# Optimization experiments

Hardware: AMD Instinct MI355X
Metric: run time of the kernel (lower is better)

## Reference

```python
import jax, jax.numpy as jnp
import numpy as np
from jax import lax

SPARSITY = 0.5  # args.sparsity: fraction of weights KEPT


def get_subnet(scores, k):
    """GetSubnet.forward: sort |scores|, zero lowest (1-k) fraction, one elsewhere."""
    sa = jnp.abs(scores)
    n = sa.size
    j = int((1.0 - k) * n)  # static: number of entries zeroed
    idx = jnp.argsort(sa.ravel())  # ascending, matches torch .sort()
    mask = jnp.zeros((n,), dtype=sa.dtype).at[idx[j:]].set(1.0)
    return mask.reshape(scores.shape)


def masked_conv(x, w, s, b, stride):
    m = get_subnet(s, SPARSITY)
    y = lax.conv_general_dilated(
        x, w * m, window_strides=(stride, stride), padding=((1, 1), (1, 1)),
        dimension_numbers=('NCHW', 'OIHW', 'NCHW'))
    return y + b[None, :, None, None]


def setup_inputs() -> dict:
    key = jax.random.key(0)
    ks = jax.random.split(key, 16)
    def rn(k, shape, scale):
        return jax.random.normal(k, shape, dtype=jnp.float32) * scale
    return {
        'x':   rn(ks[0], (64, 3, 64, 64), 1.0),
        'w1':  rn(ks[1], (128, 3, 3, 3), 0.2),   's1': rn(ks[2], (128, 3, 3, 3), 1.0),   'b1': rn(ks[3], (128,), 0.01),
        'w2':  rn(ks[4], (256, 128, 3, 3), 0.05), 's2': rn(ks[5], (256, 128, 3, 3), 1.0), 'b2': rn(ks[6], (256,), 0.01),
        'w3':  rn(ks[7], (512, 256, 3, 3), 0.03), 's3': rn(ks[8], (512, 256, 3, 3), 1.0), 'b3': rn(ks[9], (512,), 0.01),
        'fw1': rn(ks[10], (1024, 512), 0.05),     'fs1': rn(ks[11], (1024, 512), 1.0),    'fb1': rn(ks[12], (1024,), 0.01),
        'fw2': rn(ks[13], (10, 1024), 0.05),      'fs2': rn(ks[14], (10, 1024), 1.0),     'fb2': rn(ks[15], (10,), 0.01),
    }


def reference(x, w1, s1, b1, w2, s2, b2, w3, s3, b3, fw1, fs1, fb1, fw2, fs2, fb2):
    h = jax.nn.relu(masked_conv(x, w1, s1, b1, stride=1))   # [64,128,64,64]
    h = jax.nn.relu(masked_conv(h, w2, s2, b2, stride=2))   # [64,256,32,32]
    h = jax.nn.relu(masked_conv(h, w3, s3, b3, stride=2))   # [64,512,16,16]
    h = h.mean(axis=(2, 3))                                 # [64,512] global avg pool
    m1 = get_subnet(fs1, SPARSITY)
    h = jax.nn.relu(h @ (fw1 * m1).T + fb1)                 # [64,1024]
    m2 = get_subnet(fs2, SPARSITY)
    return h @ (fw2 * m2).T + fb2                           # [64,10]
```

## Files before the change

### kernel.cpp

```cpp
#include <hip/hip_runtime.h>
#include <stdint.h>


typedef __attribute__((ext_vector_type(8))) short short8;
typedef __attribute__((ext_vector_type(4))) short short4v;
typedef __attribute__((ext_vector_type(4))) float floatx4;

__device__ __forceinline__ unsigned short f2bf(float f) {
    unsigned u = __float_as_uint(f);
    u += 0x7fffu + ((u >> 16) & 1u);
    return (unsigned short)(u >> 16);
}

constexpr unsigned CUM0 = 3456u;
constexpr unsigned CUM1 = 298368u;
constexpr unsigned CUM2 = 1478016u;
constexpr unsigned CUM3 = 2002304u;
constexpr unsigned STOT = 2012544u;
constexpr int NBH = 512;

__device__ __forceinline__ int find_tensor(unsigned idx, unsigned& li) {
    if (idx < CUM0) { li = idx;        return 0; }
    if (idx < CUM1) { li = idx - CUM0; return 1; }
    if (idx < CUM2) { li = idx - CUM1; return 2; }
    if (idx < CUM3) { li = idx - CUM2; return 3; }
    li = idx - CUM3; return 4;
}

__global__ __launch_bounds__(256) void histfind(const float* __restrict__ s0,
                                                const float* __restrict__ s1,
                                                const float* __restrict__ s2,
                                                const float* __restrict__ s3,
                                                const float* __restrict__ s4,
                                                unsigned* __restrict__ ghist4,
                                                unsigned* __restrict__ done,
                                                unsigned* __restrict__ P,
                                                unsigned* __restrict__ targ,
                                                int pass) {
    __shared__ unsigned lh[4 * 1280];
    __shared__ unsigned sticket;
    const int tid = threadIdx.x;
    const int wv = tid >> 6;
    for (int i = tid; i < 4 * 1280; i += 256) lh[i] = 0;
    __syncthreads();

    const int hi_sh = 31 - 8 * pass;
    const int bin_sh = 23 - 8 * pass;
    unsigned pref[5];
    #pragma unroll
    for (int t = 0; t < 5; t++) pref[t] = pass ? P[t] : 0u;

    for (unsigned idx = blockIdx.x * 256u + tid; idx < STOT; idx += (unsigned)NBH * 256u) {
        unsigned li; int t = find_tensor(idx, li);
        const float* sp = t == 0 ? s0 : t == 1 ? s1 : t == 2 ? s2 : t == 3 ? s3 : s4;
        unsigned key = __float_as_uint(sp[li]) & 0x7fffffffu;
        if ((key >> hi_sh) == pref[t]) {
            unsigned bin = (pass == 3) ? (key & 127u) : ((key >> bin_sh) & 255u);
            atomicAdd(&lh[wv * 1280 + (unsigned)t * 256u + bin], 1u);
        }
    }
    __syncthreads();

    unsigned* gh = ghist4 + pass * 1280;
    for (int i = tid; i < 1280; i += 256) {
        unsigned v = lh[i] + lh[1280 + i] + lh[2560 + i] + lh[3840 + i];
        if (v) atomicAdd(&gh[i], v);
    }
    __syncthreads();
    if (tid == 0) {
        __threadfence();
        sticket = atomicAdd(&done[pass], 1u);
    }
    __syncthreads();

    if (sticket == (unsigned)(NBH - 1)) {
        for (int i = tid; i < 1280; i += 256)
            lh[i] = atomicAdd(&gh[i], 0u);
        __syncthreads();
        if (tid < 5) {
            int t = tid;
            unsigned n = t == 0 ? 3456u : t == 1 ? 294912u : t == 2 ? 1179648u
                       : t == 3 ? 524288u : 10240u;
            unsigned target = (pass == 0) ? (n >> 1) : targ[t];
            const unsigned* bins = &lh[t * 256];
            unsigned cum = 0; int b = 0;
            for (; b < 256; b++) { unsigned c = bins[b]; if (cum + c > target) break; cum += c; }
            targ[t] = target - cum;
            unsigned prev = (pass == 0) ? 0u : P[t];
            P[t] = (prev << ((pass == 3) ? 7 : 8)) | (unsigned)b;
        }
    }
}

__global__ void mask_reorder(const float* __restrict__ w0, const float* __restrict__ w1,
                             const float* __restrict__ w2, const float* __restrict__ w3,
                             const float* __restrict__ w4,
                             const float* __restrict__ s0, const float* __restrict__ s1,
                             const float* __restrict__ s2, const float* __restrict__ s3,
                             const float* __restrict__ s4,
                             const unsigned* __restrict__ T,
                             float* __restrict__ wm1,
                             unsigned short* __restrict__ A2,
                             unsigned short* __restrict__ A3,
                             float* __restrict__ fwm1, float* __restrict__ fwm2,
                             float* __restrict__ pooled) {
    unsigned idx = blockIdx.x * 256u + threadIdx.x;
    if (idx >= STOT) return;
    if (idx < 32768u) pooled[idx] = 0.f;
    unsigned li; int t = find_tensor(idx, li);
    const float* sp = t == 0 ? s0 : t == 1 ? s1 : t == 2 ? s2 : t == 3 ? s3 : s4;
    const float* wp = t == 0 ? w0 : t == 1 ? w1 : t == 2 ? w2 : t == 3 ? w3 : w4;
    unsigned key = __float_as_uint(sp[li]) & 0x7fffffffu;
    float val = (key >= T[t]) ? wp[li] : 0.f;
    if (t == 0) {
        wm1[li] = val;
    } else if (t == 1) {
        unsigned k = li / 1152u, r = li - k * 1152u;
        unsigned c = r / 9u, e = r - c * 9u;
        A2[((size_t)e * 256u + k) * 128u + c] = f2bf(val);
    } else if (t == 2) {
        unsigned k = li / 2304u, r = li - k * 2304u;
        unsigned c = r / 9u, e = r - c * 9u;
        A3[((size_t)e * 512u + k) * 256u + c] = f2bf(val);
    } else if (t == 3) {
        fwm1[li] = val;
    } else {
        fwm2[li] = val;
    }
}

template <int C, int H, int W, int K, int TX, int TY, int KT>
__global__ __launch_bounds__(TX* TY) void conv_direct(const float* __restrict__ in,
                                                      const float* __restrict__ wm,
                                                      const float* __restrict__ bias,
                                                      unsigned short* __restrict__ out) {
    constexpr int TILW = TX * 2, TILH = TY * 2;
    constexpr int ITW = TILW + 2, ITH = TILH + 2;
    constexpr int NTHREADS = TX * TY;
    constexpr int NLOAD = (ITH * ITW + NTHREADS - 1) / NTHREADS;
    constexpr int KG = K / KT;

    __shared__ float sIn[ITH * ITW];
    __shared__ float sW[9 * KT];

    const int tid = threadIdx.x;
    const int tx = tid % TX, ty = tid / TX;
    const int kg = blockIdx.z % KG, n = blockIdx.z / KG;
    const int ox0 = blockIdx.x * TILW, oy0 = blockIdx.y * TILH;
    const int ix0 = ox0 - 1, iy0 = oy0 - 1;

    const float* inN = in + (size_t)n * C * H * W;
    const float* wkg = wm + (size_t)kg * KT * C * 9;

    int goff[NLOAD];
    #pragma unroll
    for (int i = 0; i < NLOAD; i++) {
        int idx = tid + i * NTHREADS;
        if (idx < ITH * ITW) {
            int r = idx / ITW, col = idx % ITW;
            int gy = iy0 + r, gx = ix0 + col;
            goff[i] = (gy >= 0 && gy < H && gx >= 0 && gx < W) ? (gy * W + gx) : -1;
        } else goff[i] = -2;
    }

    float acc[2][2][KT];
    #pragma unroll
    for (int py = 0; py < 2; py++)
        #pragma unroll
        for (int px = 0; px < 2; px++)
            #pragma unroll
            for (int j = 0; j < KT; j++) acc[py][px][j] = 0.f;

    for (int c = 0; c < C; c++) {
        const float* inC = inN + (size_t)c * H * W;
        #pragma unroll
        for (int i = 0; i < NLOAD; i++) {
            int g = goff[i];
            if (g >= -1) sIn[tid + i * NTHREADS] = (g >= 0) ? inC[g] : 0.f;
        }
        for (int i = tid; i < 9 * KT; i += NTHREADS) {
            int e = i / KT, j = i % KT;
            sW[i] = wkg[j * C * 9 + c * 9 + e];
        }
        __syncthreads();

        float vin[4][4];
        const float* base = &sIn[(ty * 2) * ITW + tx * 2];
        #pragma unroll
        for (int r = 0; r < 4; r++)
            #pragma unroll
            for (int cc = 0; cc < 4; cc++) vin[r][cc] = base[r * ITW + cc];

        #pragma unroll
        for (int e = 0; e < 9; e++) {
            const int dy = e / 3, dx = e % 3;
            #pragma unroll
            for (int j = 0; j < KT; j++) {
                float wv = sW[e * KT + j];
                #pragma unroll
                for (int py = 0; py < 2; py++)
                    #pragma unroll
                    for (int px = 0; px < 2; px++)
                        acc[py][px][j] = fmaf(vin[py + dy][px + dx], wv, acc[py][px][j]);
            }
        }
        __syncthreads();
    }

    float bj[KT];
    #pragma unroll
    for (int j = 0; j < KT; j++) bj[j] = bias[kg * KT + j];
    #pragma unroll
    for (int py = 0; py < 2; py++)
        #pragma unroll
        for (int px = 0; px < 2; px++) {
            int oy = oy0 + ty * 2 + py, ox = ox0 + tx * 2 + px;
            short8 v;
            #pragma unroll
            for (int j = 0; j < KT; j++) {
                float t = acc[py][px][j] + bj[j];
                v[j] = (short)f2bf(t > 0.f ? t : 0.f);
            }
            *(short8*)(out + ((size_t)(n * H + oy) * W + ox) * K + kg * KT) = v;
        }
}

template <int C, int H, int W, int KOUT, bool POOL>
__global__ __launch_bounds__(256) void conv_mfma(const unsigned short* __restrict__ in,
                                                 const unsigned short* __restrict__ A,
                                                 const float* __restrict__ bias,
                                                 void* __restrict__ outv) {
    constexpr int OH = H / 2, OW = W / 2;
    constexpr int PR = 128 / OW;
    constexpr int RH = 2 * PR + 1;
    constexpr int IW = W + 1;
    constexpr int NC = C / 32;
    constexpr int PSTR = 40;
    constexpr int NSLOT = RH * IW * 4;
    constexpr int SLMAX = (NSLOT + 255) / 256;

    __shared__ unsigned short sIn[RH * IW * PSTR];

    const int tid = threadIdx.x;
    const int lane = tid & 63;
    const int wv = tid >> 6;
    const int l15 = lane & 15;
    const int quad = lane >> 4;
    const int pt = blockIdx.x, kb = blockIdx.y, n = blockIdx.z;
    const int k0 = kb * 128;
    const int oy0 = pt * PR;
    const int g0y = 2 * oy0 - 1;
    const int mw = wv * 32;

    int goff[SLMAX], slds[SLMAX];
    #pragma unroll
    for (int i = 0; i < SLMAX; i++) {
        int s = tid + i * 256;
        if (s < NSLOT) {
            int q = s & 3, pix = s >> 2;
            int ix = pix % IW, iy = pix / IW;
            int gy = g0y + iy, gx = ix - 1;
            slds[i] = pix * PSTR + q * 8;
            goff[i] = (gy >= 0 && gy < H && gx >= 0) ? ((gy * W + gx) * C + q * 8) : -1;
        } else { goff[i] = -2; slds[i] = 0; }
    }

    int pB[8];
    #pragma unroll
    for (int fn = 0; fn < 8; fn++) {
        int p = fn * 16 + l15;
        int oyl = p / OW, oxl = p % OW;
        pB[fn] = (oyl * 2 * IW + oxl * 2) * PSTR + quad * 8;
    }

    const unsigned short* inN = in + (size_t)n * H * W * C;

    floatx4 acc[2][8];
    #pragma unroll
    for (int fm = 0; fm < 2; fm++)
        #pragma unroll
        for (int fn = 0; fn < 8; fn++) acc[fm][fn] = (floatx4){0.f, 0.f, 0.f, 0.f};

    for (int cc = 0; cc < NC; cc++) {
        __syncthreads();
        const int cof = cc * 32;
        #pragma unroll
        for (int i = 0; i < SLMAX; i++) {
            int g = goff[i];
            if (g >= 0) {
                *(short8*)&sIn[slds[i]] = *(const short8*)(inN + g + cof);
            } else if (g == -1 && cc == 0) {
                *(short8*)&sIn[slds[i]] = (short8){0, 0, 0, 0, 0, 0, 0, 0};
            }
        }
        __syncthreads();

        const unsigned short* Abase = A + (size_t)(k0 + mw + l15) * C + cof + quad * 8;
        const size_t estr = (size_t)KOUT * C;

        short8 a0 = *(const short8*)(Abase);
        short8 a1 = *(const short8*)(Abase + 16 * C);

        #pragma unroll 1
        for (int e = 0; e < 9; e++) {
            short8 ac0 = a0, ac1 = a1;
            if (e < 8) {
                a0 = *(const short8*)(Abase + (size_t)(e + 1) * estr);
                a1 = *(const short8*)(Abase + (size_t)(e + 1) * estr + 16 * C);
            }
            const int dy = e / 3, dx = e - dy * 3;
            const int boff = (dy * IW + dx) * PSTR;
            short8 bfr[8];
            #pragma unroll
            for (int fn = 0; fn < 8; fn++)
                bfr[fn] = *(const short8*)&sIn[pB[fn] + boff];
            #pragma unroll
            for (int fn = 0; fn < 8; fn++) {
                acc[0][fn] = __builtin_amdgcn_mfma_f32_16x16x32_bf16(ac0, bfr[fn], acc[0][fn], 0, 0, 0);
                acc[1][fn] = __builtin_amdgcn_mfma_f32_16x16x32_bf16(ac1, bfr[fn], acc[1][fn], 0, 0, 0);
            }
        }
    }

    if (!POOL) {
        unsigned short* out = (unsigned short*)outv;
        #pragma unroll
        for (int fm = 0; fm < 2; fm++) {
            const int k4 = k0 + mw + fm * 16 + quad * 4;
            float b0 = bias[k4], b1 = bias[k4 + 1], b2 = bias[k4 + 2], b3 = bias[k4 + 3];
            #pragma unroll
            for (int fn = 0; fn < 8; fn++) {
                int p = fn * 16 + l15;
                int oy = oy0 + p / OW, ox = p % OW;
                float v0 = acc[fm][fn][0] + b0, v1 = acc[fm][fn][1] + b1;
                float v2 = acc[fm][fn][2] + b2, v3 = acc[fm][fn][3] + b3;
                short4v v;
                v[0] = (short)f2bf(v0 > 0.f ? v0 : 0.f);
                v[1] = (short)f2bf(v1 > 0.f ? v1 : 0.f);
                v[2] = (short)f2bf(v2 > 0.f ? v2 : 0.f);
                v[3] = (short)f2bf(v3 > 0.f ? v3 : 0.f);
                *(short4v*)(out + ((size_t)(n * OH + oy) * OW + ox) * KOUT + k4) = v;
            }
        }
    } else {
        float* out = (float*)outv;
        #pragma unroll
        for (int fm = 0; fm < 2; fm++) {
            #pragma unroll
            for (int reg = 0; reg < 4; reg++) {
                int k = k0 + mw + fm * 16 + quad * 4 + reg;
                float bv = bias[k];
                float s = 0.f;
                #pragma unroll
                for (int fn = 0; fn < 8; fn++) {
                    float v = acc[fm][fn][reg] + bv;
                    s += v > 0.f ? v : 0.f;
                }
                s += __shfl_xor(s, 1); s += __shfl_xor(s, 2);
                s += __shfl_xor(s, 4); s += __shfl_xor(s, 8);
                if (l15 == 0) atomicAdd(&out[n * KOUT + k], s * (1.0f / (OH * OW)));
            }
        }
    }
}

__global__ __launch_bounds__(256) void fc_fused(const float* __restrict__ pooled,
                                                const float* __restrict__ w1v,
                                                const float* __restrict__ b1v,
                                                const float* __restrict__ w2v,
                                                const float* __restrict__ b2v,
                                                float* __restrict__ out) {
    const int n = blockIdx.x, tid = threadIdx.x;
    __shared__ float sp[512];
    __shared__ float sh[1024];
    __shared__ float redw[40];

    {
        float2 v = *(const float2*)(pooled + (size_t)n * 512 + tid * 2);
        sp[tid * 2] = v.x; sp[tid * 2 + 1] = v.y;
    }
    __syncthreads();

    #pragma unroll
    for (int j = 0; j < 4; j++) {
        int o = tid + j * 256;
        const float4* w4 = (const float4*)(w1v + (size_t)o * 512);
        float acc = 0.f;
        for (int i = 0; i < 128; i++) {
            float4 ww = w4[i];
            acc += sp[i * 4] * ww.x + sp[i * 4 + 1] * ww.y
                 + sp[i * 4 + 2] * ww.z + sp[i * 4 + 3] * ww.w;
        }
        acc += b1v[o];
        sh[o] = acc > 0.f ? acc : 0.f;
    }
    __syncthreads();

    for (int o = 0; o < 10; o++) {
        const float4* w4 = (const float4*)(w2v + (size_t)o * 1024);
        float4 ww = w4[tid];
        float v = sh[tid * 4] * ww.x + sh[tid * 4 + 1] * ww.y
                + sh[tid * 4 + 2] * ww.z + sh[tid * 4 + 3] * ww.w;
        for (int off = 32; off > 0; off >>= 1) v += __shfl_down(v, off);
        if ((tid & 63) == 0) redw[o * 4 + (tid >> 6)] = v;
    }
    __syncthreads();
    if (tid < 10) {
        out[n * 10 + tid] = redw[tid * 4] + redw[tid * 4 + 1]
                          + redw[tid * 4 + 2] + redw[tid * 4 + 3] + b2v[tid];
    }
}

extern "C" void kernel_launch(void* const* d_in, const int* in_sizes, int n_in,
                              void* d_out, int out_size, void* d_ws, size_t ws_size,
                              hipStream_t stream) {
    const float* x   = (const float*)d_in[0];
    const float* w1  = (const float*)d_in[1];
    const float* s1  = (const float*)d_in[2];
    const float* b1  = (const float*)d_in[3];
    const float* w2  = (const float*)d_in[4];
    const float* s2  = (const float*)d_in[5];
    const float* b2  = (const float*)d_in[6];
    const float* w3  = (const float*)d_in[7];
    const float* s3  = (const float*)d_in[8];
    const float* b3  = (const float*)d_in[9];
    const float* fw1 = (const float*)d_in[10];
    const float* fs1 = (const float*)d_in[11];
    const float* fb1 = (const float*)d_in[12];
    const float* fw2 = (const float*)d_in[13];
    const float* fs2 = (const float*)d_in[14];
    const float* fb2 = (const float*)d_in[15];
    float* out = (float*)d_out;

    char* ws = (char*)d_ws;
    size_t off = 0;
    auto alloc = [&](size_t bytes) -> char* {
        char* p = ws + off;
        off = (off + bytes + 255) & ~(size_t)255;
        return p;
    };
    unsigned* ghist = (unsigned*)alloc((4 * 1280 + 16) * 4);
    unsigned* done  = ghist + 4 * 1280;
    unsigned* P     = (unsigned*)alloc(64);
    unsigned* targ  = (unsigned*)alloc(64);
    float* wm1  = (float*)alloc(3456ull * 4);
    float* fwm1 = (float*)alloc(524288ull * 4);
    float* fwm2 = (float*)alloc(10240ull * 4);
    unsigned short* A2 = (unsigned short*)alloc(294912ull * 2);
    unsigned short* A3 = (unsigned short*)alloc(1179648ull * 2);
    unsigned short* h1 = (unsigned short*)alloc(33554432ull * 2);
    unsigned short* h2 = (unsigned short*)alloc(16777216ull * 2);
    float* pooled = (float*)alloc(32768ull * 4);
    if (off > ws_size) return;

    (void)hipMemsetAsync(ghist, 0, (4 * 1280 + 16) * 4, stream);

    for (int pass = 0; pass < 4; pass++)
        histfind<<<NBH, 256, 0, stream>>>(s1, s2, s3, fs1, fs2, ghist, done, P, targ, pass);

    int gs = (STOT + 255) / 256;
    mask_reorder<<<gs, 256, 0, stream>>>(w1, w2, w3, fw1, fw2, s1, s2, s3, fs1, fs2, P,
                                         wm1, A2, A3, fwm1, fwm2, pooled);

    conv_direct<3, 64, 64, 128, 16, 16, 8>
        <<<dim3(2, 2, 64 * 16), 256, 0, stream>>>(x, wm1, b1, h1);
    conv_mfma<128, 64, 64, 256, false>
        <<<dim3(8, 2, 64), 256, 0, stream>>>(h1, A2, b2, h2);
    conv_mfma<256, 32, 32, 512, true>
        <<<dim3(2, 4, 64), 256, 0, stream>>>(h2, A3, b3, pooled);

    fc_fused<<<64, 256, 0, stream>>>(pooled, fwm1, fb1, fwm2, fb2, out);
}
```

Before: 469.3 us.

## Split histogram radix-select into separate hist and find kernels, fewer blocks

After: 482.9 us. 1.03x slower.

```diff
diff --git a/kernel.cpp b/kernel.cpp
--- a/kernel.cpp
+++ b/kernel.cpp
@@ -17,7 +17,7 @@
 constexpr unsigned CUM2 = 1478016u;
 constexpr unsigned CUM3 = 2002304u;
 constexpr unsigned STOT = 2012544u;
-constexpr int NBH = 512;
+constexpr int NBH = 128;
 
 __device__ __forceinline__ int find_tensor(unsigned idx, unsigned& li) {
     if (idx < CUM0) { li = idx;        return 0; }
@@ -27,18 +27,14 @@
     li = idx - CUM3; return 4;
 }
 
-__global__ __launch_bounds__(256) void histfind(const float* __restrict__ s0,
-                                                const float* __restrict__ s1,
-                                                const float* __restrict__ s2,
-                                                const float* __restrict__ s3,
-                                                const float* __restrict__ s4,
-                                                unsigned* __restrict__ ghist4,
-                                                unsigned* __restrict__ done,
-                                                unsigned* __restrict__ P,
-                                                unsigned* __restrict__ targ,
-                                                int pass) {
+__global__ __launch_bounds__(256) void hist8(const float* __restrict__ s0,
+                                             const float* __restrict__ s1,
+                                             const float* __restrict__ s2,
+                                             const float* __restrict__ s3,
+                                             const float* __restrict__ s4,
+                                             const unsigned* __restrict__ P,
+                                             unsigned* __restrict__ ghist4, int pass) {
     __shared__ unsigned lh[4 * 1280];
-    __shared__ unsigned sticket;
     const int tid = threadIdx.x;
     const int wv = tid >> 6;
     for (int i = tid; i < 4 * 1280; i += 256) lh[i] = 0;
@@ -50,7 +46,7 @@
     #pragma unroll
     for (int t = 0; t < 5; t++) pref[t] = pass ? P[t] : 0u;
 
-    for (unsigned idx = blockIdx.x * 256u + tid; idx < STOT; idx += (unsigned)NBH * 256u) {
+    for (unsigned idx = blockIdx.x * 256u + tid; idx < STOT; idx += NBH * 256u) {
         unsigned li; int t = find_tensor(idx, li);
         const float* sp = t == 0 ? s0 : t == 1 ? s1 : t == 2 ? s2 : t == 3 ? s3 : s4;
         unsigned key = __float_as_uint(sp[li]) & 0x7fffffffu;
@@ -60,35 +56,30 @@
         }
     }
     __syncthreads();
-
     unsigned* gh = ghist4 + pass * 1280;
     for (int i = tid; i < 1280; i += 256) {
         unsigned v = lh[i] + lh[1280 + i] + lh[2560 + i] + lh[3840 + i];
         if (v) atomicAdd(&gh[i], v);
     }
+}
+
+__global__ __launch_bounds__(256) void find8(const unsigned* __restrict__ ghist4,
+                                             unsigned* __restrict__ P,
+                                             unsigned* __restrict__ targ, int pass) {
+    const int t = blockIdx.x;
+    const int tid = threadIdx.x;
+    __shared__ unsigned bins[256];
+    bins[tid] = ghist4[pass * 1280 + t * 256 + tid];
     __syncthreads();
     if (tid == 0) {
-        __threadfence();
-        sticket = atomicAdd(&done[pass], 1u);
-    }
-    __syncthreads();
-
-    if (sticket == (unsigned)(NBH - 1)) {
-        for (int i = tid; i < 1280; i += 256)
-            lh[i] = atomicAdd(&gh[i], 0u);
-        __syncthreads();
-        if (tid < 5) {
-            int t = tid;
-            unsigned n = t == 0 ? 3456u : t == 1 ? 294912u : t == 2 ? 1179648u
-                       : t == 3 ? 524288u : 10240u;
-            unsigned target = (pass == 0) ? (n >> 1) : targ[t];
-            const unsigned* bins = &lh[t * 256];
-            unsigned cum = 0; int b = 0;
-            for (; b < 256; b++) { unsigned c = bins[b]; if (cum + c > target) break; cum += c; }
-            targ[t] = target - cum;
-            unsigned prev = (pass == 0) ? 0u : P[t];
-            P[t] = (prev << ((pass == 3) ? 7 : 8)) | (unsigned)b;
-        }
+        unsigned n = t == 0 ? 3456u : t == 1 ? 294912u : t == 2 ? 1179648u
+                   : t == 3 ? 524288u : 10240u;
+        unsigned target = (pass == 0) ? (n >> 1) : targ[t];
+        unsigned cum = 0; int b = 0;
+        for (; b < 256; b++) { unsigned c = bins[b]; if (cum + c > target) break; cum += c; }
+        targ[t] = target - cum;
+        unsigned prev = (pass == 0) ? 0u : P[t];
+        P[t] = (prev << ((pass == 3) ? 7 : 8)) | (unsigned)b;
     }
 }
 
@@ -439,8 +430,7 @@
         off = (off + bytes + 255) & ~(size_t)255;
         return p;
     };
-    unsigned* ghist = (unsigned*)alloc((4 * 1280 + 16) * 4);
-    unsigned* done  = ghist + 4 * 1280;
+    unsigned* ghist = (unsigned*)alloc(4ull * 1280 * 4);
     unsigned* P     = (unsigned*)alloc(64);
     unsigned* targ  = (unsigned*)alloc(64);
     float* wm1  = (float*)alloc(3456ull * 4);
@@ -453,11 +443,12 @@
     float* pooled = (float*)alloc(32768ull * 4);
     if (off > ws_size) return;
 
-    (void)hipMemsetAsync(ghist, 0, (4 * 1280 + 16) * 4, stream);
-
-    for (int pass = 0; pass < 4; pass++)
-        histfind<<<NBH, 256, 0, stream>>>(s1, s2, s3, fs1, fs2, ghist, done, P, targ, pass);
-
+    (void)hipMemsetAsync(ghist, 0, 4ull * 1280 * 4, stream);
+
+    for (int pass = 0; pass < 4; pass++) {
+        hist8<<<NBH, 256, 0, stream>>>(s1, s2, s3, fs1, fs2, P, ghist, pass);
+        find8<<<5, 256, 0, stream>>>(ghist, P, targ, pass);
+    }
     int gs = (STOT + 255) / 256;
     mask_reorder<<<gs, 256, 0, stream>>>(w1, w2, w3, fw1, fw2, s1, s2, s3, fs1, fs2, P,
                                          wm1, A2, A3, fwm1, fwm2, pooled);
```
